# Performance work log

Measured on AMD Instinct MI355X. Metric: run time of the kernel, lower is better.

Reference implementation:

```python
import jax, jax.numpy as jnp
import numpy as np


def _gcn(h, W, b, src, dst):
    # PyG GCNConv: x @ W, then symmetric-normalized aggregation over edges
    # (edge list already includes self-loops), bias added after.
    n = h.shape[0]
    deg = jnp.zeros((n,), h.dtype).at[dst].add(jnp.ones((), h.dtype))
    dinv = jnp.where(deg > 0, jax.lax.rsqrt(deg), jnp.zeros((), h.dtype))
    norm = dinv[src] * dinv[dst]  # [E]
    m = h @ W                     # [N, d_h]
    out = jnp.zeros_like(m).at[dst].add(norm[:, None] * m[src])
    return out + b


def setup_inputs() -> dict:
    key = jax.random.key(0)
    F, K = 1000, 100              # files, blocks per file
    N = F * K                     # total blocks
    D_SEM, D_STR = 768, 256
    D_H, D_SH, D_PR, NPROJ = 512, 256, 256, 100

    # sliding-window (window=2) edges within each file, bidirectional, + self loops
    base = np.arange(N)
    pos = base % K
    s_l, d_l = [], []
    for d in (1, 2):
        i = base[pos < K - d]
        j = i + d
        s_l += [i, j]
        d_l += [j, i]
    s_l.append(base)  # self loops (GCNConv add_self_loops)
    d_l.append(base)
    src = jnp.asarray(np.concatenate(s_l), dtype=jnp.int32)
    dst = jnp.asarray(np.concatenate(d_l), dtype=jnp.int32)
    seg_ids = jnp.asarray(base // K, dtype=jnp.int32)  # file id per block (CSR blk_ptr equivalent)

    ks = jax.random.split(key, 16)
    def w(k, shape):
        return jax.random.normal(k, shape, jnp.float32) * 0.02
    z = lambda n: jnp.zeros((n,), jnp.float32)

    return dict(
        h_sem=jax.random.normal(ks[0], (N, D_SEM), jnp.float32),
        e_struct=jax.random.normal(ks[1], (N, D_STR), jnp.float32),
        W_fusion=w(ks[2], (D_SEM + D_STR, D_H)), b_fusion=z(D_H),
        W_g1=w(ks[3], (D_H, D_H)), b_g1=z(D_H),
        W_g2=w(ks[4], (D_H, D_H)), b_g2=z(D_H),
        W_att=w(ks[5], (D_H, D_H)), b_att=z(D_H),
        context=w(ks[6], (D_H,)),
        W_sh1=w(ks[7], (D_H, D_SH)), b_sh1=z(D_SH),
        W_sh2=w(ks[8], (D_SH, D_SH)), b_sh2=z(D_SH),
        W_pr1=w(ks[9], (D_H, D_PR)), b_pr1=z(D_PR),
        W_pr2=w(ks[10], (D_PR, D_PR)), b_pr2=z(D_PR),
        W_dpr=w(ks[11], (D_PR, NPROJ)), b_dpr=z(NPROJ),
        W_bug=w(ks[12], (D_H, 1)), b_bug=z(1),
        src=src, dst=dst, seg_ids=seg_ids, num_files=F,
    )


def reference(h_sem, e_struct, W_fusion, b_fusion, W_g1, b_g1, W_g2, b_g2,
              W_att, b_att, context, W_sh1, b_sh1, W_sh2, b_sh2,
              W_pr1, b_pr1, W_pr2, b_pr2, W_dpr, b_dpr, W_bug, b_bug,
              src, dst, seg_ids, num_files):
    # fusion of semantic + structural features
    h0 = jnp.concatenate([h_sem, e_struct], axis=1) @ W_fusion + b_fusion  # [N, d_h]
    h1 = jax.nn.relu(_gcn(h0, W_g1, b_g1, src, dst))
    h_blk = _gcn(h1, W_g2, b_g2, src, dst)                                # [N, d_h]

    # ragged attention pooling over per-file segments (vectorized segment softmax)
    scores = jnp.tanh(h_blk @ W_att + b_att) @ context                    # [N]
    seg_max = jax.ops.segment_max(scores, seg_ids, num_segments=num_files)
    ex = jnp.exp(scores - seg_max[seg_ids])
    seg_sum = jax.ops.segment_sum(ex, seg_ids, num_segments=num_files)
    alpha = ex / seg_sum[seg_ids]                                         # [N]
    h_file = jax.ops.segment_sum(alpha[:, None] * h_blk, seg_ids,
                                 num_segments=num_files)                  # [F, d_h]

    z_sh = jax.nn.relu(h_file @ W_sh1 + b_sh1) @ W_sh2 + b_sh2            # [F, d_sh]
    z_pr = jax.nn.relu(h_file @ W_pr1 + b_pr1) @ W_pr2 + b_pr2            # [F, d_pr]
    logits_pr_dom = z_pr @ W_dpr + b_dpr                                  # [F, num_projects]
    logit_bug = h_file @ W_bug + b_bug                                    # [F, 1]
    loss_ortho = jnp.mean((z_sh.T @ z_pr) ** 2)                           # disentanglement penalty
    return (h_blk, alpha, h_file, z_sh, z_pr, logits_pr_dom, logit_bug, loss_ortho)
```

## Files before the change

kernel.cpp:

```cpp
#include <hip/hip_runtime.h>

typedef unsigned short u16;
typedef unsigned int   u32;
typedef __attribute__((ext_vector_type(8))) short  short8;
typedef __attribute__((ext_vector_type(4))) float  floatx4;

#define DEV __device__ __forceinline__

DEV float bf2f(u16 u){ return __uint_as_float(((u32)u) << 16); }
DEV u16 f2bf(float x){
  u32 u = __float_as_uint(x);
  u += 0x7FFFu + ((u >> 16) & 1u);
  return (u16)(u >> 16);
}
DEV float blo(u32 u){ return __uint_as_float(u << 16); }
DEV float bhi(u32 u){ return __uint_as_float(u & 0xffff0000u); }

DEV void async16(const void* g, void* l){
  __builtin_amdgcn_global_load_lds((__attribute__((address_space(1))) void*)g,
                                   (__attribute__((address_space(3))) void*)l,
                                   16, 0, 0);
}

constexpr int NN   = 100000;
constexpr int FF   = 1000;
constexpr int KPF  = 100;
constexpr int DH   = 512;

constexpr size_t OUT_HBLK  = 0;
constexpr size_t OUT_ALPHA = 51200000;
constexpr size_t OUT_HFILE = 51300000;
constexpr size_t OUT_ZSH   = 51812000;
constexpr size_t OUT_ZPR   = 52068000;
constexpr size_t OUT_LOG   = 52324000;
constexpr size_t OUT_BUG   = 52424000;
constexpr size_t OUT_LOSS  = 52425000;

constexpr size_t WS_A      = 0;
constexpr size_t WS_M1     = 0;
constexpr size_t WS_H1     = 102400000;
constexpr size_t WS_HBLK   = 0;
constexpr size_t WS_H0     = 204800000;
constexpr size_t WS_M2     = 204800000;
constexpr size_t WS_SCOREP = 307200000;
constexpr size_t WS_WT     = 308800000;
constexpr size_t WS_HFILEB = 312300000;
constexpr size_t WS_TSH    = 313400000;
constexpr size_t WS_TPR    = 314000000;
constexpr size_t WS_ZPRB   = 314600000;
constexpr size_t WS_ORTHOP = 315200000;

constexpr int WT_FUS = 0;
constexpr int WT_G1  = 524288;
constexpr int WT_G2  = 786432;
constexpr int WT_ATT = 1048576;
constexpr int WT_SH1 = 1310720;
constexpr int WT_SH2 = 1441792;
constexpr int WT_PR1 = 1507328;
constexpr int WT_PR2 = 1638400;
constexpr int WT_DPR = 1703936;
constexpr int WT_TOT = 1729536;

struct PrepTab {
  const float* src[9];
  int K[9];
  int N[9];
  int prefix[10];
};

__global__ __launch_bounds__(256) void prep_w(PrepTab t, u16* __restrict__ dst){
  int gid = blockIdx.x * 256 + threadIdx.x;
  if (gid >= t.prefix[9]) return;
  int i = 0;
  while (gid >= t.prefix[i+1]) ++i;
  int e  = gid - t.prefix[i];
  int Ni = t.N[i];
  int k  = e / Ni;
  int n  = e - k * Ni;
  dst[t.prefix[i] + (size_t)n * t.K[i] + k] = f2bf(t.src[i][(size_t)k * Ni + n]);
}

__global__ __launch_bounds__(256) void build_A(const float* __restrict__ hsem,
                                               const float* __restrict__ est,
                                               u16* __restrict__ out){
  int gid = blockIdx.x * 256 + threadIdx.x;
  int row = gid >> 7;
  int c   = (gid & 127) << 3;
  const float* src = (c < 768) ? (hsem + (size_t)row * 768 + c)
                               : (est  + (size_t)row * 256 + (c - 768));
  float4 v0 = *(const float4*)src;
  float4 v1 = *(const float4*)(src + 4);
  uint4 o;
  o.x = (u32)f2bf(v0.x) | ((u32)f2bf(v0.y) << 16);
  o.y = (u32)f2bf(v0.z) | ((u32)f2bf(v0.w) << 16);
  o.z = (u32)f2bf(v1.x) | ((u32)f2bf(v1.y) << 16);
  o.w = (u32)f2bf(v1.z) | ((u32)f2bf(v1.w) << 16);
  *(uint4*)(out + (size_t)row * 1024 + c) = o;
}

template<int MODE, bool BIAS, bool RELU>
__global__ __launch_bounds__(256) void gemm_bt(
    const u16* __restrict__ A, const u16* __restrict__ B,
    int M, int N, int K, int ny,
    const float* __restrict__ bias,
    u16* __restrict__ outb, float* __restrict__ outf,
    int ldc, int nvalid,
    const float* __restrict__ ctx, float* __restrict__ scorep)
{
  __shared__ u16 As[3 * 4096];
  __shared__ u16 Bs[3 * 4096];
  const int tid  = threadIdx.x;
  const int wave = tid >> 6, lane = tid & 63;

  const int nwg = (int)gridDim.x;
  const int q   = nwg >> 3, r = nwg & 7;
  const int xcd = (int)blockIdx.x & 7, pos = (int)blockIdx.x >> 3;
  const int lid = (xcd < r ? xcd * (q + 1) : r * (q + 1) + (xcd - r) * q) + pos;
  const int ty  = lid % ny, tx = lid / ny;
  const int m0  = tx << 7, n0 = ty << 7;

  const int wm = (wave & 1) << 6, wn = (wave >> 1) << 6;
  const int lq = lane >> 4, lr = lane & 15;

  floatx4 acc[4][4];
  #pragma unroll
  for (int i = 0; i < 4; ++i)
    #pragma unroll
    for (int j = 0; j < 4; ++j)
      acc[i][j] = floatx4{0.f, 0.f, 0.f, 0.f};

  int arow = m0 + (wave << 4) + (lane >> 2);
  int ar0 = min(arow, M - 1);
  int ar1 = min(arow + 64, M - 1);
  int brow = n0 + (wave << 4) + (lane >> 2);
  int br0 = min(brow, N - 1);
  int br1 = min(brow + 64, N - 1);
  const int kc = (((lane & 3) ^ ((lane >> 3) & 3)) << 3);
  const u16* ga0 = A + (size_t)ar0 * K + kc;
  const u16* ga1 = A + (size_t)ar1 * K + kc;
  const u16* gb0 = B + (size_t)br0 * K + kc;
  const u16* gb1 = B + (size_t)br1 * K + kc;

  auto STAGE = [&](int buf){
    u16* as = As + (buf << 12);
    u16* bs = Bs + (buf << 12);
    async16(ga0, as + (wave << 9));
    async16(ga1, as + 2048 + (wave << 9));
    async16(gb0, bs + (wave << 9));
    async16(gb1, bs + 2048 + (wave << 9));
    ga0 += 32; ga1 += 32; gb0 += 32; gb1 += 32;
  };

  const int nIt = K >> 5;
  STAGE(0);
  if (nIt > 1) STAGE(1);
  const int rsw = (lr >> 1) & 3;
  int bt = 0;
  for (int it = 0; it < nIt; ++it) {
    if (it + 1 < nIt) asm volatile("s_waitcnt vmcnt(4) lgkmcnt(0)" ::: "memory");
    else              asm volatile("s_waitcnt vmcnt(0) lgkmcnt(0)" ::: "memory");
    __builtin_amdgcn_s_barrier();
    __builtin_amdgcn_sched_barrier(0);
    if (it + 2 < nIt) { int b2 = bt + 2; if (b2 >= 3) b2 -= 3; STAGE(b2); }
    const u16* as = As + (bt << 12);
    const u16* bs = Bs + (bt << 12);
    short8 af[4], bfr[4];
    #pragma unroll
    for (int mi = 0; mi < 4; ++mi)
      af[mi] = *(const short8*)(as + ((wm + mi * 16 + lr) << 5) + ((lq ^ rsw) << 3));
    #pragma unroll
    for (int ni = 0; ni < 4; ++ni)
      bfr[ni] = *(const short8*)(bs + ((wn + ni * 16 + lr) << 5) + ((lq ^ rsw) << 3));
    #pragma unroll
    for (int mi = 0; mi < 4; ++mi)
      #pragma unroll
      for (int ni = 0; ni < 4; ++ni)
        acc[mi][ni] = __builtin_amdgcn_mfma_f32_16x16x32_bf16(af[mi], bfr[ni], acc[mi][ni], 0, 0, 0);
    if (++bt == 3) bt = 0;
  }

  if constexpr (MODE == 3) {
    #pragma unroll
    for (int mi = 0; mi < 4; ++mi) {
      #pragma unroll
      for (int r2 = 0; r2 < 4; ++r2) {
        float p = 0.f;
        #pragma unroll
        for (int ni = 0; ni < 4; ++ni) {
          int gc = n0 + wn + ni * 16 + lr;
          p += tanhf(acc[mi][ni][r2] + bias[gc]) * ctx[gc];
        }
        p += __shfl_xor(p, 1); p += __shfl_xor(p, 2);
        p += __shfl_xor(p, 4); p += __shfl_xor(p, 8);
        int gr = m0 + wm + mi * 16 + lq * 4 + r2;
        if (lr == 0 && gr < M) scorep[(size_t)ty * M + gr] = p;
      }
    }
  } else {
    #pragma unroll
    for (int mi = 0; mi < 4; ++mi) {
      int grb = m0 + wm + mi * 16 + lq * 4;
      #pragma unroll
      for (int ni = 0; ni < 4; ++ni) {
        int gc = n0 + wn + ni * 16 + lr;
        if (gc >= nvalid) continue;
        float bv = BIAS ? bias[gc] : 0.f;
        #pragma unroll
        for (int r2 = 0; r2 < 4; ++r2) {
          int gr = grb + r2;
          if (gr >= M) continue;
          float v = acc[mi][ni][r2] + bv;
          if (RELU) v = fmaxf(v, 0.f);
          if (MODE == 0 || MODE == 2) outb[(size_t)gr * ldc + gc] = f2bf(v);
          if (MODE == 1 || MODE == 2) outf[(size_t)gr * ldc + gc] = v;
        }
      }
    }
  }
}

DEV float dinv_of(int p){
  return rsqrtf((float)(1 + min(p, 2) + min(99 - p, 2)));
}

template<bool RELU, bool DUAL>
__global__ __launch_bounds__(256) void agg_k(const u16* __restrict__ m,
                                             const float* __restrict__ bias,
                                             u16* __restrict__ outb,
                                             float* __restrict__ outf){
  int gid = blockIdx.x * 256 + threadIdx.x;
  int row = gid >> 6;
  int c   = (gid & 63) << 3;
  int pos = row % KPF;
  float ds = dinv_of(pos);
  float a0=0,a1=0,a2=0,a3=0,a4=0,a5=0,a6=0,a7=0;
  #pragma unroll
  for (int d = -2; d <= 2; ++d) {
    int p2 = pos + d;
    if (p2 < 0 || p2 >= KPF) continue;
    float w = ds * dinv_of(p2);
    uint4 v = *(const uint4*)(m + (size_t)(row + d) * DH + c);
    a0 += w * blo(v.x); a1 += w * bhi(v.x);
    a2 += w * blo(v.y); a3 += w * bhi(v.y);
    a4 += w * blo(v.z); a5 += w * bhi(v.z);
    a6 += w * blo(v.w); a7 += w * bhi(v.w);
  }
  float o[8] = {a0,a1,a2,a3,a4,a5,a6,a7};
  #pragma unroll
  for (int j = 0; j < 8; ++j) {
    o[j] += bias[c + j];
    if (RELU) o[j] = fmaxf(o[j], 0.f);
  }
  uint4 st;
  st.x = (u32)f2bf(o[0]) | ((u32)f2bf(o[1]) << 16);
  st.y = (u32)f2bf(o[2]) | ((u32)f2bf(o[3]) << 16);
  st.z = (u32)f2bf(o[4]) | ((u32)f2bf(o[5]) << 16);
  st.w = (u32)f2bf(o[6]) | ((u32)f2bf(o[7]) << 16);
  *(uint4*)(outb + (size_t)row * DH + c) = st;
  if (DUAL) {
    float4 f0 = {o[0], o[1], o[2], o[3]};
    float4 f1 = {o[4], o[5], o[6], o[7]};
    *(float4*)(outf + (size_t)row * DH + c)     = f0;
    *(float4*)(outf + (size_t)row * DH + c + 4) = f1;
  }
}

__global__ __launch_bounds__(256) void pool_k(const float* __restrict__ sp,
                                              const u16* __restrict__ hblk,
                                              float* __restrict__ alpha_out,
                                              float* __restrict__ hfile_f,
                                              u16* __restrict__ hfile_b){
  int f = blockIdx.x, tid = threadIdx.x;
  __shared__ float sAl[KPF];
  __shared__ float red[8];
  float s = -INFINITY;
  if (tid < KPF) {
    int r = f * KPF + tid;
    s = sp[r] + sp[NN + r] + sp[2 * NN + r] + sp[3 * NN + r];
  }
  float mx = s;
  for (int off = 32; off >= 1; off >>= 1) mx = fmaxf(mx, __shfl_xor(mx, off));
  if ((tid & 63) == 0) red[tid >> 6] = mx;
  __syncthreads();
  mx = fmaxf(fmaxf(red[0], red[1]), fmaxf(red[2], red[3]));
  float ex = (tid < KPF) ? expf(s - mx) : 0.f;
  float sm = ex;
  for (int off = 32; off >= 1; off >>= 1) sm += __shfl_xor(sm, off);
  if ((tid & 63) == 0) red[4 + (tid >> 6)] = sm;
  __syncthreads();
  sm = red[4] + red[5] + red[6] + red[7];
  float al = ex / sm;
  if (tid < KPF) { alpha_out[(size_t)f * KPF + tid] = al; sAl[tid] = al; }
  __syncthreads();
  const u16* base = hblk + (size_t)f * KPF * DH;
  float acc0 = 0.f, acc1 = 0.f;
  for (int i = 0; i < KPF; ++i) {
    float w = sAl[i];
    acc0 += w * bf2f(base[i * DH + tid]);
    acc1 += w * bf2f(base[i * DH + 256 + tid]);
  }
  hfile_f[(size_t)f * DH + tid]       = acc0;
  hfile_f[(size_t)f * DH + 256 + tid] = acc1;
  hfile_b[(size_t)f * DH + tid]       = f2bf(acc0);
  hfile_b[(size_t)f * DH + 256 + tid] = f2bf(acc1);
}

__global__ __launch_bounds__(256) void bug_k(const float* __restrict__ hfile,
                                             const float* __restrict__ w,
                                             const float* __restrict__ b,
                                             float* __restrict__ out){
  int row  = blockIdx.x * 4 + (threadIdx.x >> 6);
  int lane = threadIdx.x & 63;
  const float* h = hfile + (size_t)row * DH;
  float s = 0.f;
  #pragma unroll
  for (int j = 0; j < 8; ++j) s += h[lane + j * 64] * w[lane + j * 64];
  for (int off = 32; off >= 1; off >>= 1) s += __shfl_xor(s, off);
  if (lane == 0) out[row] = s + b[0];
}

__global__ __launch_bounds__(256) void ortho_k(const float* __restrict__ zsh,
                                               const float* __restrict__ zpr,
                                               float* __restrict__ part){
  int bi = blockIdx.x >> 4, bj = blockIdx.x & 15;
  int ty = threadIdx.x >> 4, tx = threadIdx.x & 15;
  __shared__ float sa[64 * 16], sb[64 * 16];
  float acc = 0.f;
  for (int k0 = 0; k0 < FF; k0 += 64) {
    #pragma unroll
    for (int q = 0; q < 4; ++q) {
      int kk = ty + q * 16;
      int k  = k0 + kk;
      float va = 0.f, vb = 0.f;
      if (k < FF) {
        va = zsh[(size_t)k * 256 + bi * 16 + tx];
        vb = zpr[(size_t)k * 256 + bj * 16 + tx];
      }
      sa[kk * 16 + tx] = va;
      sb[kk * 16 + tx] = vb;
    }
    __syncthreads();
    #pragma unroll 8
    for (int kk = 0; kk < 64; ++kk) acc += sa[kk * 16 + ty] * sb[kk * 16 + tx];
    __syncthreads();
  }
  float ssq = acc * acc;
  for (int off = 32; off >= 1; off >>= 1) ssq += __shfl_xor(ssq, off);
  __shared__ float r[4];
  if ((threadIdx.x & 63) == 0) r[threadIdx.x >> 6] = ssq;
  __syncthreads();
  if (threadIdx.x == 0) part[blockIdx.x] = r[0] + r[1] + r[2] + r[3];
}

__global__ __launch_bounds__(256) void ortho_fin(const float* __restrict__ part,
                                                 float* __restrict__ out){
  int tid = threadIdx.x;
  float s = part[tid];
  for (int off = 32; off >= 1; off >>= 1) s += __shfl_xor(s, off);
  __shared__ float r[4];
  if ((tid & 63) == 0) r[tid >> 6] = s;
  __syncthreads();
  if (tid == 0) out[0] = (r[0] + r[1] + r[2] + r[3]) * (1.0f / 65536.0f);
}

extern "C" void kernel_launch(void* const* d_in, const int* in_sizes, int n_in,
                              void* d_out, int out_size, void* d_ws, size_t ws_size,
                              hipStream_t stream) {
  const float* h_sem    = (const float*)d_in[0];
  const float* e_struct = (const float*)d_in[1];
  const float* W_fusion = (const float*)d_in[2];
  const float* b_fusion = (const float*)d_in[3];
  const float* W_g1     = (const float*)d_in[4];
  const float* b_g1     = (const float*)d_in[5];
  const float* W_g2     = (const float*)d_in[6];
  const float* b_g2     = (const float*)d_in[7];
  const float* W_att    = (const float*)d_in[8];
  const float* b_att    = (const float*)d_in[9];
  const float* context  = (const float*)d_in[10];
  const float* W_sh1    = (const float*)d_in[11];
  const float* b_sh1    = (const float*)d_in[12];
  const float* W_sh2    = (const float*)d_in[13];
  const float* b_sh2    = (const float*)d_in[14];
  const float* W_pr1    = (const float*)d_in[15];
  const float* b_pr1    = (const float*)d_in[16];
  const float* W_pr2    = (const float*)d_in[17];
  const float* b_pr2    = (const float*)d_in[18];
  const float* W_dpr    = (const float*)d_in[19];
  const float* b_dpr    = (const float*)d_in[20];
  const float* W_bug    = (const float*)d_in[21];
  const float* b_bug    = (const float*)d_in[22];

  char*  ws  = (char*)d_ws;
  float* out = (float*)d_out;

  u16*   Abf    = (u16*)(ws + WS_A);
  u16*   h0b    = (u16*)(ws + WS_H0);
  u16*   m1b    = (u16*)(ws + WS_M1);
  u16*   h1b    = (u16*)(ws + WS_H1);
  u16*   m2b    = (u16*)(ws + WS_M2);
  u16*   hblkb  = (u16*)(ws + WS_HBLK);
  float* scorep = (float*)(ws + WS_SCOREP);
  u16*   WT     = (u16*)(ws + WS_WT);
  u16*   hfileb = (u16*)(ws + WS_HFILEB);
  u16*   tshb   = (u16*)(ws + WS_TSH);
  u16*   tprb   = (u16*)(ws + WS_TPR);
  u16*   zprb   = (u16*)(ws + WS_ZPRB);
  float* opart  = (float*)(ws + WS_ORTHOP);

  PrepTab t;
  const float* srcs[9] = {W_fusion, W_g1, W_g2, W_att, W_sh1, W_sh2, W_pr1, W_pr2, W_dpr};
  int Ks[9] = {1024, 512, 512, 512, 512, 256, 512, 256, 256};
  int Ns[9] = {512, 512, 512, 512, 256, 256, 256, 256, 100};
  int pre[10] = {WT_FUS, WT_G1, WT_G2, WT_ATT, WT_SH1, WT_SH2, WT_PR1, WT_PR2, WT_DPR, WT_TOT};
  for (int i = 0; i < 9; ++i) { t.src[i] = srcs[i]; t.K[i] = Ks[i]; t.N[i] = Ns[i]; }
  for (int i = 0; i < 10; ++i) t.prefix[i] = pre[i];
  prep_w<<<(WT_TOT + 255) / 256, 256, 0, stream>>>(t, WT);

  build_A<<<NN * 128 / 256, 256, 0, stream>>>(h_sem, e_struct, Abf);

  gemm_bt<0, true, false><<<782 * 4, 256, 0, stream>>>(
      Abf, WT + WT_FUS, NN, 512, 1024, 4, b_fusion, h0b, nullptr, 512, 512, nullptr, nullptr);

  gemm_bt<0, false, false><<<782 * 4, 256, 0, stream>>>(
      h0b, WT + WT_G1, NN, 512, 512, 4, nullptr, m1b, nullptr, 512, 512, nullptr, nullptr);

  agg_k<true, false><<<NN * 64 / 256, 256, 0, stream>>>(m1b, b_g1, h1b, nullptr);

  gemm_bt<0, false, false><<<782 * 4, 256, 0, stream>>>(
      h1b, WT + WT_G2, NN, 512, 512, 4, nullptr, m2b, nullptr, 512, 512, nullptr, nullptr);

  agg_k<false, true><<<NN * 64 / 256, 256, 0, stream>>>(m2b, b_g2, hblkb, out + OUT_HBLK);

  gemm_bt<3, true, false><<<782 * 4, 256, 0, stream>>>(
      hblkb, WT + WT_ATT, NN, 512, 512, 4, b_att, nullptr, nullptr, 512, 512, context, scorep);

  pool_k<<<FF, 256, 0, stream>>>(scorep, hblkb, out + OUT_ALPHA, out + OUT_HFILE, hfileb);

  gemm_bt<0, true, true><<<8 * 2, 256, 0, stream>>>(
      hfileb, WT + WT_SH1, FF, 256, 512, 2, b_sh1, tshb, nullptr, 256, 256, nullptr, nullptr);
  gemm_bt<1, true, false><<<8 * 2, 256, 0, stream>>>(
      tshb, WT + WT_SH2, FF, 256, 256, 2, b_sh2, nullptr, out + OUT_ZSH, 256, 256, nullptr, nullptr);
  gemm_bt<0, true, true><<<8 * 2, 256, 0, stream>>>(
      hfileb, WT + WT_PR1, FF, 256, 512, 2, b_pr1, tprb, nullptr, 256, 256, nullptr, nullptr);
  gemm_bt<2, true, false><<<8 * 2, 256, 0, stream>>>(
      tprb, WT + WT_PR2, FF, 256, 256, 2, b_pr2, zprb, out + OUT_ZPR, 256, 256, nullptr, nullptr);
  gemm_bt<1, true, false><<<8 * 1, 256, 0, stream>>>(
      zprb, WT + WT_DPR, FF, 100, 256, 1, b_dpr, nullptr, out + OUT_LOG, 100, 100, nullptr, nullptr);

  bug_k<<<FF / 4, 256, 0, stream>>>(out + OUT_HFILE, W_bug, b_bug, out + OUT_BUG);

  ortho_k<<<256, 256, 0, stream>>>(out + OUT_ZSH, out + OUT_ZPR, opart);
  ortho_fin<<<1, 256, 0, stream>>>(opart, out + OUT_LOSS);
}
```

Measured before the change: 1.377 ms.

## Replace large GEMMs with 256x256-tile 512-thread MFMA kernel

Adds a gemm256 kernel that uses 256x256 output tiles with 8 waves, double-buffered async global-to-LDS loads in 128KB of dynamic shared memory, and an XOR-swizzled LDS layout. It replaces the four big N=100000 GEMMs, including the attention-score epilogue. With two column tiles the score partials become 2 instead of 4, so pool_k is updated to match. Larger tiles increase operand reuse and cut redundant A reads, at the cost of heavy register use and 128KB of LDS, which may limit occupancy. The bf16 epilogue stores are scalar per element, which may be less efficient than before.

```diff
diff --git a/kernel.cpp b/kernel.cpp
--- a/kernel.cpp
+++ b/kernel.cpp
@@ -96,6 +96,133 @@
   o.z = (u32)f2bf(v1.x) | ((u32)f2bf(v1.y) << 16);
   o.w = (u32)f2bf(v1.z) | ((u32)f2bf(v1.w) << 16);
   *(uint4*)(out + (size_t)row * 1024 + c) = o;
+}
+
+template<int MODE, bool BIAS>
+__global__ __launch_bounds__(512, 2) void gemm256(
+    const u16* __restrict__ A, const u16* __restrict__ B,
+    int M, int N, int K,
+    const float* __restrict__ bias,
+    u16* __restrict__ outb,
+    const float* __restrict__ ctx, float* __restrict__ scorep)
+{
+  extern __shared__ u16 S[];
+  const int tid  = threadIdx.x;
+  const int wid  = tid >> 6, lane = tid & 63;
+  const int lq   = lane >> 4, lr = lane & 15;
+
+  const int ny  = N >> 8;
+  const int nwg = (int)gridDim.x;
+  const int q   = nwg >> 3, r = nwg & 7;
+  const int xcd = (int)blockIdx.x & 7, pos = (int)blockIdx.x >> 3;
+  const int lid = (xcd < r ? xcd * (q + 1) : r * (q + 1) + (xcd - r) * q) + pos;
+  const int ty  = lid % ny, tx = lid / ny;
+  const int m0  = tx << 8, n0 = ty << 8;
+
+  const int wr = wid >> 2, wc = wid & 3;
+  const int wrow = wr << 7, wcol = wc << 6;
+
+  const int srow = (wid << 3) + (lane >> 3);
+  const int scol = ((lane & 7) ^ (lane >> 3)) << 3;
+  const u16* pa[4];
+  const u16* pb[4];
+  #pragma unroll
+  for (int h = 0; h < 2; ++h)
+    #pragma unroll
+    for (int j = 0; j < 2; ++j) {
+      int ra = m0 + h * 128 + j * 64 + srow;  ra = min(ra, M - 1);
+      int rb = n0 + h * 128 + j * 64 + srow;
+      pa[h * 2 + j] = A + (size_t)ra * K + scol;
+      pb[h * 2 + j] = B + (size_t)rb * K + scol;
+    }
+
+  auto STAGE = [&](int p){
+    char* base = (char*)S + (p << 16) + (wid << 10);
+    #pragma unroll
+    for (int h = 0; h < 2; ++h)
+      #pragma unroll
+      for (int j = 0; j < 2; ++j) {
+        async16(pa[h * 2 + j], base + h * 16384 + j * 8192);
+        async16(pb[h * 2 + j], base + 32768 + h * 16384 + j * 8192);
+        pa[h * 2 + j] += 64;  pb[h * 2 + j] += 64;
+      }
+  };
+
+  floatx4 acc[8][4];
+  #pragma unroll
+  for (int i = 0; i < 8; ++i)
+    #pragma unroll
+    for (int j = 0; j < 4; ++j)
+      acc[i][j] = floatx4{0.f, 0.f, 0.f, 0.f};
+
+  const int NT = K >> 6;
+  STAGE(0);
+  STAGE(1);
+
+  const int rsl = lr & 7;
+  for (int kt = 0; kt < NT; ++kt) {
+    if (kt + 1 < NT) asm volatile("s_waitcnt vmcnt(8)" ::: "memory");
+    else             asm volatile("s_waitcnt vmcnt(0)" ::: "memory");
+    __builtin_amdgcn_s_barrier();
+    __builtin_amdgcn_sched_barrier(0);
+    const u16* ap = S + ((kt & 1) << 15);
+    const u16* bp = ap + 16384;
+    #pragma unroll
+    for (int k2 = 0; k2 < 2; ++k2) {
+      short8 af[8], bf[4];
+      const int sl = ((k2 << 2) | lq) ^ rsl;
+      #pragma unroll
+      for (int mi = 0; mi < 8; ++mi)
+        af[mi] = *(const short8*)(ap + ((wrow + mi * 16 + lr) << 6) + (sl << 3));
+      #pragma unroll
+      for (int ni = 0; ni < 4; ++ni)
+        bf[ni] = *(const short8*)(bp + ((wcol + ni * 16 + lr) << 6) + (sl << 3));
+      __builtin_amdgcn_s_setprio(1);
+      #pragma unroll
+      for (int mi = 0; mi < 8; ++mi)
+        #pragma unroll
+        for (int ni = 0; ni < 4; ++ni)
+          acc[mi][ni] = __builtin_amdgcn_mfma_f32_16x16x32_bf16(af[mi], bf[ni], acc[mi][ni], 0, 0, 0);
+      __builtin_amdgcn_s_setprio(0);
+    }
+    __builtin_amdgcn_s_barrier();
+    __builtin_amdgcn_sched_barrier(0);
+    if (kt + 2 < NT) STAGE(kt & 1);
+  }
+
+  if constexpr (MODE == 3) {
+    #pragma unroll
+    for (int mi = 0; mi < 8; ++mi) {
+      #pragma unroll
+      for (int r2 = 0; r2 < 4; ++r2) {
+        float psum = 0.f;
+        #pragma unroll
+        for (int ni = 0; ni < 4; ++ni) {
+          int gc = n0 + wcol + ni * 16 + lr;
+          psum += tanhf(acc[mi][ni][r2] + bias[gc]) * ctx[gc];
+        }
+        psum += __shfl_xor(psum, 1); psum += __shfl_xor(psum, 2);
+        psum += __shfl_xor(psum, 4); psum += __shfl_xor(psum, 8);
+        int gr = m0 + wrow + mi * 16 + (lq << 2) + r2;
+        if (lr == 0 && gr < M) scorep[(size_t)ty * M + gr] = psum;
+      }
+    }
+  } else {
+    #pragma unroll
+    for (int mi = 0; mi < 8; ++mi) {
+      int grb = m0 + wrow + mi * 16 + (lq << 2);
+      #pragma unroll
+      for (int ni = 0; ni < 4; ++ni) {
+        int gc = n0 + wcol + ni * 16 + lr;
+        float bv = BIAS ? bias[gc] : 0.f;
+        #pragma unroll
+        for (int r2 = 0; r2 < 4; ++r2) {
+          int gr = grb + r2;
+          if (gr < M) outb[(size_t)gr * N + gc] = f2bf(acc[mi][ni][r2] + bv);
+        }
+      }
+    }
+  }
 }
 
 template<int MODE, bool BIAS, bool RELU>
@@ -276,7 +403,7 @@
   float s = -INFINITY;
   if (tid < KPF) {
     int r = f * KPF + tid;
-    s = sp[r] + sp[NN + r] + sp[2 * NN + r] + sp[3 * NN + r];
+    s = sp[r] + sp[NN + r];
   }
   float mx = s;
   for (int off = 32; off >= 1; off >>= 1) mx = fmaxf(mx, __shfl_xor(mx, off));
@@ -418,21 +545,21 @@
 
   build_A<<<NN * 128 / 256, 256, 0, stream>>>(h_sem, e_struct, Abf);
 
-  gemm_bt<0, true, false><<<782 * 4, 256, 0, stream>>>(
-      Abf, WT + WT_FUS, NN, 512, 1024, 4, b_fusion, h0b, nullptr, 512, 512, nullptr, nullptr);
-
-  gemm_bt<0, false, false><<<782 * 4, 256, 0, stream>>>(
-      h0b, WT + WT_G1, NN, 512, 512, 4, nullptr, m1b, nullptr, 512, 512, nullptr, nullptr);
+  gemm256<0, true><<<391 * 2, 512, 131072, stream>>>(
+      Abf, WT + WT_FUS, NN, 512, 1024, b_fusion, h0b, nullptr, nullptr);
+
+  gemm256<0, false><<<391 * 2, 512, 131072, stream>>>(
+      h0b, WT + WT_G1, NN, 512, 512, nullptr, m1b, nullptr, nullptr);
 
   agg_k<true, false><<<NN * 64 / 256, 256, 0, stream>>>(m1b, b_g1, h1b, nullptr);
 
-  gemm_bt<0, false, false><<<782 * 4, 256, 0, stream>>>(
-      h1b, WT + WT_G2, NN, 512, 512, 4, nullptr, m2b, nullptr, 512, 512, nullptr, nullptr);
+  gemm256<0, false><<<391 * 2, 512, 131072, stream>>>(
+      h1b, WT + WT_G2, NN, 512, 512, nullptr, m2b, nullptr, nullptr);
 
   agg_k<false, true><<<NN * 64 / 256, 256, 0, stream>>>(m2b, b_g2, hblkb, out + OUT_HBLK);
 
-  gemm_bt<3, true, false><<<782 * 4, 256, 0, stream>>>(
-      hblkb, WT + WT_ATT, NN, 512, 512, 4, b_att, nullptr, nullptr, 512, 512, context, scorep);
+  gemm256<3, true><<<391 * 2, 512, 131072, stream>>>(
+      hblkb, WT + WT_ATT, NN, 512, 512, b_att, nullptr, context, scorep);
 
   pool_k<<<FF, 256, 0, stream>>>(scorep, hblkb, out + OUT_ALPHA, out + OUT_HFILE, hfileb);
 
```

New measurement: 1.462 ms. 1.06x slower.
